# Performance work log

Hardware: AMD Instinct MI355X
Metric: run time of the kernel (lower is better)

Reference implementation:

```python
import jax, jax.numpy as jnp
import numpy as np

B, C, H, W, N = 4, 5, 256, 256, 2048
HW = H * W


def setup_inputs() -> dict:
    key = jax.random.key(0)
    ks = jax.random.split(key, 8)
    s = 1.0 / np.sqrt(C)
    x = jax.random.normal(ks[0], (B, C, H, W), jnp.float32)
    Wq = jax.random.normal(ks[1], (C, C), jnp.float32) * s
    Wk = jax.random.normal(ks[2], (C, C), jnp.float32) * s
    Wv = jax.random.normal(ks[3], (C, C), jnp.float32) * s
    bq = jnp.zeros((C,), jnp.float32)
    bk = jnp.zeros((C,), jnp.float32)
    bv = jnp.zeros((C,), jnp.float32)
    gamma = jnp.zeros((1,), jnp.float32)  # nn.Parameter(torch.zeros(1))
    idx_b = jax.random.randint(ks[4], (N,), 0, B, jnp.int32)
    idx_h = jax.random.randint(ks[5], (N,), 0, H, jnp.int32)
    idx_w = jax.random.randint(ks[6], (N,), 0, W, jnp.int32)
    return {"x": x, "Wq": Wq, "bq": bq, "Wk": Wk, "bk": bk, "Wv": Wv,
            "bv": bv, "gamma": gamma, "idx_b": idx_b, "idx_h": idx_h, "idx_w": idx_w}


def _conv1x1(x, Wt, b):
    # 1x1 conv == per-pixel channel mix
    return jnp.einsum('oc,bchw->bohw', Wt, x) + b[None, :, None, None]


def reference(x, Wq, bq, Wk, bk, Wv, bv, gamma, idx_b, idx_h, idx_w):
    q = _conv1x1(x, Wq, bq)
    k = _conv1x1(x, Wk, bk)
    v = _conv1x1(x, Wv, bv)
    q_pix = q[idx_b, :, idx_h, idx_w]              # [N, C] gathered query pixels
    Kf = k.reshape(B, C, HW)
    Vf = v.reshape(B, C, HW)
    # energy[n, l] = sum_c q_pix[n, c] * Kf[idx_b[n], c, l]
    # channel loop (C=5, fixed) avoids materializing [N, C, HW]
    energy = jnp.zeros((N, HW), x.dtype)
    for c in range(C):
        energy = energy + q_pix[:, c:c + 1] * Kf[idx_b, c]   # [N, HW]
    attn = jax.nn.softmax(energy, axis=-1)                   # [N, HW]
    out = jnp.stack([jnp.sum(Vf[idx_b, c] * attn, axis=-1) for c in range(C)],
                    axis=1)                                  # [N, C]
    upd = (gamma[0] + 0.1) * out + x[idx_b, :, idx_h, idx_w]
    # y starts as a detached copy of x; selected pixels are overwritten
    y = jax.lax.stop_gradient(x).at[idx_b, :, idx_h, idx_w].set(upd)
    return y
```

## Files before the change

kernel.cpp:

```cpp
#include <hip/hip_runtime.h>


constexpr int HWC = 256 * 256;
constexpr int Bc  = 4;
constexpr int Nq  = 2048;
constexpr int Wc  = 256;

constexpr int TPB   = 40;
constexpr int SPLIT = 16;

constexpr float LOG2E = 1.4426950408889634f;
constexpr float BIAS2 = -14.0f * LOG2E;

constexpr size_t K8_BYTES  = (size_t)Bc * HWC * 8 * 2;
constexpr size_t VT_BYTES  = (size_t)Bc * 5 * HWC * 2;
constexpr size_t QP_BYTES  = (size_t)Nq * 8 * 2;
constexpr size_t PART_BYTES = (size_t)SPLIT * Nq * 6 * 4;
constexpr size_t K8_OFF   = 0;
constexpr size_t VT_OFF   = K8_OFF + K8_BYTES;
constexpr size_t QP16_OFF = VT_OFF + VT_BYTES;
constexpr size_t PART_OFF = QP16_OFF + QP_BYTES;
constexpr size_t PERM_OFF = PART_OFF + PART_BYTES;
constexpr size_t CNT_OFF  = PERM_OFF + (size_t)Bc * Nq * 4;

typedef __attribute__((ext_vector_type(8))) _Float16 f16x8;
typedef __attribute__((ext_vector_type(4))) float f32x4;
union FU { uint4 u; f16x8 h; };

#if defined(__has_builtin)
#if __has_builtin(__builtin_amdgcn_exp2f)
#define EXP2F(x) __builtin_amdgcn_exp2f(x)
#endif
#endif
#ifndef EXP2F
#define EXP2F(x) exp2f(x)
#endif

__device__ inline unsigned pack2(float a, float b) {
  typedef __attribute__((ext_vector_type(2))) __fp16 fp16x2;
  union { fp16x2 h; unsigned u; } r;
  r.h = __builtin_amdgcn_cvt_pkrtz(a, b);
  return r.u;
}

__global__ __launch_bounds__(256) void k1_prep(
    const float* __restrict__ x,
    const float* __restrict__ Wq, const float* __restrict__ bq,
    const float* __restrict__ Wk, const float* __restrict__ bk,
    const float* __restrict__ Wv, const float* __restrict__ bv,
    const int* __restrict__ idx_b, const int* __restrict__ idx_h,
    const int* __restrict__ idx_w,
    float* __restrict__ y, char* __restrict__ wsb) {
  const int tid = threadIdx.x;
  _Float16* K8   = (_Float16*)(wsb + K8_OFF);
  _Float16* VT   = (_Float16*)(wsb + VT_OFF);
  _Float16* QP16 = (_Float16*)(wsb + QP16_OFF);
  if (blockIdx.x >= 1024) {
    if (blockIdx.x == 1032) {
      __shared__ int lcnt[Bc];
      if (tid < Bc) lcnt[tid] = 0;
      __syncthreads();
      int* perm = (int*)(wsb + PERM_OFF);
#pragma unroll
      for (int qi = 0; qi < 8; ++qi) {
        const int n = qi * 256 + tid;
        const int b = idx_b[n];
        const int pos = atomicAdd(&lcnt[b], 1);
        perm[b * Nq + pos] = n;
      }
      __syncthreads();
      if (tid < Bc) ((int*)(wsb + CNT_OFF))[tid] = lcnt[tid];
      return;
    }
    const int n = (blockIdx.x - 1024) * 256 + tid;
    const int b = idx_b[n];
    const int s = idx_h[n] * Wc + idx_w[n];
    float xv[5];
#pragma unroll
    for (int c = 0; c < 5; ++c) xv[c] = x[(size_t)(b * 5 + c) * HWC + s];
    float q[5];
#pragma unroll
    for (int o = 0; o < 5; ++o) {
      float t = bq[o];
#pragma unroll
      for (int c = 0; c < 5; ++c) t = fmaf(Wq[o * 5 + c], xv[c], t);
      q[o] = t * LOG2E;
    }
    uint4 row;
    row.x = pack2(q[0], q[1]);
    row.y = pack2(q[2], q[3]);
    row.z = pack2(q[4], 0.f);
    row.w = 0u;
    *(uint4*)(QP16 + (size_t)n * 8) = row;
    return;
  }
  const int gid = blockIdx.x * 256 + tid;
  const int b   = gid >> 16;
  const int s   = gid & (HWC - 1);
  float xv[5];
#pragma unroll
  for (int c = 0; c < 5; ++c) {
    const size_t off = (size_t)(b * 5 + c) * HWC + s;
    xv[c] = x[off];
    y[off] = xv[c];
  }
  float kk[5], vv[5];
#pragma unroll
  for (int o = 0; o < 5; ++o) {
    kk[o] = bk[o];
    vv[o] = bv[o];
#pragma unroll
    for (int c = 0; c < 5; ++c) {
      kk[o] = fmaf(Wk[o * 5 + c], xv[c], kk[o]);
      vv[o] = fmaf(Wv[o * 5 + c], xv[c], vv[o]);
    }
  }
  uint4 krow;
  krow.x = pack2(kk[0], kk[1]);
  krow.y = pack2(kk[2], kk[3]);
  krow.z = pack2(kk[4], 0.f);
  krow.w = 0u;
  *(uint4*)(K8 + (size_t)(b * HWC + s) * 8) = krow;
#pragma unroll
  for (int c = 0; c < 5; ++c)
    VT[(size_t)(b * 5 + c) * HWC + s] = (_Float16)vv[c];
}

#define BODY(KC0, KC1, KC2, KC3, KN0, KN1, KN2, KN3, VN0, VN1,                \
             NBASE, DOPV, DOLOAD, RPW, WPW)                                   \
  do {                                                                        \
    f32x4 e0 = __builtin_amdgcn_mfma_f32_16x16x32_f16(KC0.h, qf.h, bias, 0, 0, 0); \
    f32x4 e1 = __builtin_amdgcn_mfma_f32_16x16x32_f16(KC1.h, qf.h, bias, 0, 0, 0); \
    f32x4 e2 = __builtin_amdgcn_mfma_f32_16x16x32_f16(KC2.h, qf.h, bias, 0, 0, 0); \
    f32x4 e3 = __builtin_amdgcn_mfma_f32_16x16x32_f16(KC3.h, qf.h, bias, 0, 0, 0); \
    if (DOPV) {                                                               \
      FU pa0, pa1;                                                            \
      pa0.h = *(const f16x8*)((RPW) + roff0);                                 \
      pa1.h = *(const f16x8*)((RPW) + roff1);                                 \
      oacc = __builtin_amdgcn_mfma_f32_16x16x32_f16(pa0.h, VN0.h, oacc, 0, 0, 0); \
      oacc = __builtin_amdgcn_mfma_f32_16x16x32_f16(pa1.h, VN1.h, oacc, 0, 0, 0); \
    }                                                                         \
    if (DOLOAD) {                                                             \
      if (quad == 0) {                                                        \
        KN0.u = *(const uint4*)(K8b + (size_t)((NBASE) +  0 + l15) * 8);      \
        KN1.u = *(const uint4*)(K8b + (size_t)((NBASE) + 16 + l15) * 8);      \
        KN2.u = *(const uint4*)(K8b + (size_t)((NBASE) + 32 + l15) * 8);      \
        KN3.u = *(const uint4*)(K8b + (size_t)((NBASE) + 48 + l15) * 8);      \
      }                                                                       \
      if (l15 < 5) {                                                          \
        VN0.u = *(const uint4*)(vplane + (NBASE) +  0 + 8 * quad);            \
        VN1.u = *(const uint4*)(vplane + (NBASE) + 32 + 8 * quad);            \
      }                                                                       \
    }                                                                         \
    uint2 w0, w1, w2, w3;                                                     \
    w0.x = pack2(EXP2F(e0.x), EXP2F(e0.y)); w0.y = pack2(EXP2F(e0.z), EXP2F(e0.w)); \
    w1.x = pack2(EXP2F(e1.x), EXP2F(e1.y)); w1.y = pack2(EXP2F(e1.z), EXP2F(e1.w)); \
    w2.x = pack2(EXP2F(e2.x), EXP2F(e2.y)); w2.y = pack2(EXP2F(e2.z), EXP2F(e2.w)); \
    w3.x = pack2(EXP2F(e3.x), EXP2F(e3.y)); w3.y = pack2(EXP2F(e3.z), EXP2F(e3.w)); \
    *(uint2*)((WPW) + woff0) = w0;                                            \
    *(uint2*)((WPW) + woff1) = w1;                                            \
    *(uint2*)((WPW) + woff2) = w2;                                            \
    *(uint2*)((WPW) + woff3) = w3;                                            \
  } while (0)

__global__ __launch_bounds__(256, 4) void k2_attn(char* __restrict__ wsb) {
  const int chunk = blockIdx.x;
  const int tile  = blockIdx.y;
  const int bb    = tile / TPB;
  const int tt    = tile % TPB;
  const int cb    = ((const int*)(wsb + CNT_OFF))[bb];
  const int j0    = tt * 16;
  if (j0 >= cb) return;
  const int* perm = (const int*)(wsb + PERM_OFF) + bb * Nq;

  const int tid  = threadIdx.x;
  const int wv   = tid >> 6;
  const int lane = tid & 63;
  const int quad = lane >> 4;
  const int l15  = lane & 15;

  __shared__ _Float16 Pbuf[4][2][16][64];
  __shared__ float    Ored[4][16][6];

  const _Float16* K8b  = (const _Float16*)(wsb + K8_OFF) + (size_t)bb * HWC * 8;
  const _Float16* Vtb  = (const _Float16*)(wsb + VT_OFF) + (size_t)bb * 5 * HWC;
  const _Float16* QP16 = (const _Float16*)(wsb + QP16_OFF);

  _Float16* PwE = &Pbuf[wv][0][0][0];
  _Float16* PwO = &Pbuf[wv][1][0][0];
  const int swzg = 2 * (l15 & 7);
  const int rowb = l15 << 6;
  const int woff0 = rowb + (((0 * 4 + quad) ^ swzg) << 2);
  const int woff1 = rowb + (((1 * 4 + quad) ^ swzg) << 2);
  const int woff2 = rowb + (((2 * 4 + quad) ^ swzg) << 2);
  const int woff3 = rowb + (((3 * 4 + quad) ^ swzg) << 2);
  const int roff0 = rowb + (((0 + 2 * quad) ^ swzg) << 2);
  const int roff1 = rowb + (((8 + 2 * quad) ^ swzg) << 2);

  FU qf; qf.u = make_uint4(0u, 0u, 0u, 0u);
  {
    const int jq = j0 + l15;
    if (quad == 0) {
      const int n = (jq < cb) ? perm[jq] : 0;
      qf.u = *(const uint4*)(QP16 + (size_t)n * 8);
    }
  }
  FU vA0, vA1, vB0, vB1;
  {
    const unsigned ones = (l15 == 5) ? 0x3C003C00u : 0u;
    vA0.u = make_uint4(ones, ones, ones, ones);
    vA1.u = vA0.u; vB0.u = vA0.u; vB1.u = vA0.u;
  }
  FU kA0, kA1, kA2, kA3, kB0, kB1, kB2, kB3;
  kA0.u = make_uint4(0u, 0u, 0u, 0u);
  kA1.u = kA0.u; kA2.u = kA0.u; kA3.u = kA0.u;
  kB0.u = kA0.u; kB1.u = kA0.u; kB2.u = kA0.u; kB3.u = kA0.u;

  const f32x4 bias = {BIAS2, BIAS2, BIAS2, BIAS2};
  f32x4 oacc = {0.f, 0.f, 0.f, 0.f};

  const _Float16* vplane = Vtb + (size_t)l15 * HWC;

  const int s0 = chunk * (HWC / SPLIT) + wv * (HWC / SPLIT / 4);

  if (quad == 0) {
    kA0.u = *(const uint4*)(K8b + (size_t)(s0 +  0 + l15) * 8);
    kA1.u = *(const uint4*)(K8b + (size_t)(s0 + 16 + l15) * 8);
    kA2.u = *(const uint4*)(K8b + (size_t)(s0 + 32 + l15) * 8);
    kA3.u = *(const uint4*)(K8b + (size_t)(s0 + 48 + l15) * 8);
  }
  if (l15 < 5) {
    vA0.u = *(const uint4*)(vplane + s0 +  0);
    vA1.u = *(const uint4*)(vplane + s0 + 32);
  }
  if (l15 < 5 && quad != 0) {
    vA0.u = *(const uint4*)(vplane + s0 +  0 + 8 * quad);
    vA1.u = *(const uint4*)(vplane + s0 + 32 + 8 * quad);
  }

  BODY(kA0, kA1, kA2, kA3, kB0, kB1, kB2, kB3, vB0, vB1,
       s0 + 64, false, true, PwE, PwE);
#pragma unroll
  for (int p = 0; p < 7; ++p) {
    const int it = 1 + 2 * p;
    BODY(kB0, kB1, kB2, kB3, kA0, kA1, kA2, kA3, vA0, vA1,
         s0 + 64 * (it + 1), true, true, PwE, PwO);
    BODY(kA0, kA1, kA2, kA3, kB0, kB1, kB2, kB3, vB0, vB1,
         s0 + 64 * (it + 2), true, true, PwO, PwE);
  }
  BODY(kB0, kB1, kB2, kB3, kA0, kA1, kA2, kA3, vA0, vA1,
       0, true, false, PwE, PwO);
  {
    FU pa0, pa1;
    pa0.h = *(const f16x8*)(PwO + roff0);
    pa1.h = *(const f16x8*)(PwO + roff1);
    oacc = __builtin_amdgcn_mfma_f32_16x16x32_f16(pa0.h, vB0.h, oacc, 0, 0, 0);
    oacc = __builtin_amdgcn_mfma_f32_16x16x32_f16(pa1.h, vB1.h, oacc, 0, 0, 0);
  }

  if (l15 < 6) {
    Ored[wv][4 * quad + 0][l15] = oacc.x;
    Ored[wv][4 * quad + 1][l15] = oacc.y;
    Ored[wv][4 * quad + 2][l15] = oacc.z;
    Ored[wv][4 * quad + 3][l15] = oacc.w;
  }
  __syncthreads();
  if (tid < 96) {
    const int q = tid / 6, comp = tid % 6;
    const float s = Ored[0][q][comp] + Ored[1][q][comp] +
                    Ored[2][q][comp] + Ored[3][q][comp];
    const int j = j0 + q;
    if (j < cb) {
      const int n = perm[j];
      ((float*)(wsb + PART_OFF))[((size_t)chunk * Nq + n) * 6 + comp] = s;
    }
  }
}

__global__ __launch_bounds__(256) void k3_final(
    const float* __restrict__ x, const float* __restrict__ gamma,
    const int* __restrict__ idx_b, const int* __restrict__ idx_h,
    const int* __restrict__ idx_w, float* __restrict__ y,
    const char* __restrict__ wsb) {
  const int n = blockIdx.x * 256 + threadIdx.x;
  const float* part = (const float*)(wsb + PART_OFF);
  float l = 0.f, o[5] = {0.f, 0.f, 0.f, 0.f, 0.f};
#pragma unroll
  for (int ch = 0; ch < SPLIT; ++ch) {
    const float* p = part + ((size_t)ch * Nq + n) * 6;
#pragma unroll
    for (int c = 0; c < 5; ++c) o[c] += p[c];
    l += p[5];
  }
  const float gsc = gamma[0] + 0.1f;
  const float inv = 1.0f / l;
  const int b = idx_b[n], h = idx_h[n], w = idx_w[n];
  const int s = h * Wc + w;
#pragma unroll
  for (int c = 0; c < 5; ++c) {
    const size_t off = (size_t)(b * 5 + c) * HWC + s;
    y[off] = fmaf(gsc, o[c] * inv, x[off]);
  }
}

extern "C" void kernel_launch(void* const* d_in, const int* in_sizes, int n_in,
                              void* d_out, int out_size, void* d_ws, size_t ws_size,
                              hipStream_t stream) {
  const float* x     = (const float*)d_in[0];
  const float* Wq    = (const float*)d_in[1];
  const float* bq    = (const float*)d_in[2];
  const float* Wk    = (const float*)d_in[3];
  const float* bk    = (const float*)d_in[4];
  const float* Wv    = (const float*)d_in[5];
  const float* bv    = (const float*)d_in[6];
  const float* gamma = (const float*)d_in[7];
  const int* idx_b   = (const int*)d_in[8];
  const int* idx_h   = (const int*)d_in[9];
  const int* idx_w   = (const int*)d_in[10];
  float* y  = (float*)d_out;
  char* wsb = (char*)d_ws;

  k1_prep<<<1033, 256, 0, stream>>>(x, Wq, bq, Wk, bk, Wv, bv,
                                    idx_b, idx_h, idx_w, y, wsb);
  k2_attn<<<dim3(SPLIT, Bc * TPB), 256, 0, stream>>>(wsb);
  k3_final<<<Nq / 256, 256, 0, stream>>>(x, gamma, idx_b, idx_h, idx_w, y, wsb);
}
```

Baseline: 118.6 us.

## Process four query tiles per block to reuse each K/V load across 64 queries

Each attention block now handles 64 queries (four 16-query groups with separate accumulators) instead of 16. Every K and V fragment loaded from global memory is reused across four MFMA groups, cutting K/V traffic roughly fourfold. SPLIT doubles to 32 so the grid stays large enough to fill the GPU. The cost is more registers, longer serial work per block, and twice as many partial results for the final reduction kernel.

```diff
diff --git a/kernel.cpp b/kernel.cpp
--- a/kernel.cpp
+++ b/kernel.cpp
@@ -6,8 +6,8 @@
 constexpr int Nq  = 2048;
 constexpr int Wc  = 256;
 
-constexpr int TPB   = 40;
-constexpr int SPLIT = 16;
+constexpr int QG    = 10;
+constexpr int SPLIT = 32;
 
 constexpr float LOG2E = 1.4426950408889634f;
 constexpr float BIAS2 = -14.0f * LOG2E;
@@ -126,30 +126,32 @@
     VT[(size_t)(b * 5 + c) * HWC + s] = (_Float16)vv[c];
 }
 
-#define BODY(KC0, KC1, KC2, KC3, KN0, KN1, KN2, KN3, VN0, VN1,                \
-             NBASE, DOPV, DOLOAD, RPW, WPW)                                   \
+#define STEP(KC0, KC1, KC2, KC3, QF, DOPV, OACC, RPW, WPW,                    \
+             DOLV, VBASE, DOLK, KD0, KD1, KD2, KD3, KBASE)                    \
   do {                                                                        \
-    f32x4 e0 = __builtin_amdgcn_mfma_f32_16x16x32_f16(KC0.h, qf.h, bias, 0, 0, 0); \
-    f32x4 e1 = __builtin_amdgcn_mfma_f32_16x16x32_f16(KC1.h, qf.h, bias, 0, 0, 0); \
-    f32x4 e2 = __builtin_amdgcn_mfma_f32_16x16x32_f16(KC2.h, qf.h, bias, 0, 0, 0); \
-    f32x4 e3 = __builtin_amdgcn_mfma_f32_16x16x32_f16(KC3.h, qf.h, bias, 0, 0, 0); \
+    f32x4 e0 = __builtin_amdgcn_mfma_f32_16x16x32_f16(KC0.h, QF.h, bias, 0, 0, 0); \
+    f32x4 e1 = __builtin_amdgcn_mfma_f32_16x16x32_f16(KC1.h, QF.h, bias, 0, 0, 0); \
+    f32x4 e2 = __builtin_amdgcn_mfma_f32_16x16x32_f16(KC2.h, QF.h, bias, 0, 0, 0); \
+    f32x4 e3 = __builtin_amdgcn_mfma_f32_16x16x32_f16(KC3.h, QF.h, bias, 0, 0, 0); \
     if (DOPV) {                                                               \
       FU pa0, pa1;                                                            \
       pa0.h = *(const f16x8*)((RPW) + roff0);                                 \
       pa1.h = *(const f16x8*)((RPW) + roff1);                                 \
-      oacc = __builtin_amdgcn_mfma_f32_16x16x32_f16(pa0.h, VN0.h, oacc, 0, 0, 0); \
-      oacc = __builtin_amdgcn_mfma_f32_16x16x32_f16(pa1.h, VN1.h, oacc, 0, 0, 0); \
+      OACC = __builtin_amdgcn_mfma_f32_16x16x32_f16(pa0.h, v0.h, OACC, 0, 0, 0); \
+      OACC = __builtin_amdgcn_mfma_f32_16x16x32_f16(pa1.h, v1.h, OACC, 0, 0, 0); \
     }                                                                         \
-    if (DOLOAD) {                                                             \
+    if (DOLV) {                                                               \
+      if (l15 < 5) {                                                          \
+        v0.u = *(const uint4*)(vplane + (VBASE) +  0 + 8 * quad);             \
+        v1.u = *(const uint4*)(vplane + (VBASE) + 32 + 8 * quad);             \
+      }                                                                       \
+    }                                                                         \
+    if (DOLK) {                                                               \
       if (quad == 0) {                                                        \
-        KN0.u = *(const uint4*)(K8b + (size_t)((NBASE) +  0 + l15) * 8);      \
-        KN1.u = *(const uint4*)(K8b + (size_t)((NBASE) + 16 + l15) * 8);      \
-        KN2.u = *(const uint4*)(K8b + (size_t)((NBASE) + 32 + l15) * 8);      \
-        KN3.u = *(const uint4*)(K8b + (size_t)((NBASE) + 48 + l15) * 8);      \
-      }                                                                       \
-      if (l15 < 5) {                                                          \
-        VN0.u = *(const uint4*)(vplane + (NBASE) +  0 + 8 * quad);            \
-        VN1.u = *(const uint4*)(vplane + (NBASE) + 32 + 8 * quad);            \
+        KD0.u = *(const uint4*)(K8b + (size_t)((KBASE) +  0 + l15) * 8);      \
+        KD1.u = *(const uint4*)(K8b + (size_t)((KBASE) + 16 + l15) * 8);      \
+        KD2.u = *(const uint4*)(K8b + (size_t)((KBASE) + 32 + l15) * 8);      \
+        KD3.u = *(const uint4*)(K8b + (size_t)((KBASE) + 48 + l15) * 8);      \
       }                                                                       \
     }                                                                         \
     uint2 w0, w1, w2, w3;                                                     \
@@ -166,10 +168,10 @@
 __global__ __launch_bounds__(256, 4) void k2_attn(char* __restrict__ wsb) {
   const int chunk = blockIdx.x;
   const int tile  = blockIdx.y;
-  const int bb    = tile / TPB;
-  const int tt    = tile % TPB;
+  const int bb    = tile / QG;
+  const int tg    = tile % QG;
   const int cb    = ((const int*)(wsb + CNT_OFF))[bb];
-  const int j0    = tt * 16;
+  const int j0    = tg * 64;
   if (j0 >= cb) return;
   const int* perm = (const int*)(wsb + PERM_OFF) + bb * Nq;
 
@@ -180,7 +182,7 @@
   const int l15  = lane & 15;
 
   __shared__ _Float16 Pbuf[4][2][16][64];
-  __shared__ float    Ored[4][16][6];
+  __shared__ float    Ored[4][4][16][6];
 
   const _Float16* K8b  = (const _Float16*)(wsb + K8_OFF) + (size_t)bb * HWC * 8;
   const _Float16* Vtb  = (const _Float16*)(wsb + VT_OFF) + (size_t)bb * 5 * HWC;
@@ -197,19 +199,24 @@
   const int roff0 = rowb + (((0 + 2 * quad) ^ swzg) << 2);
   const int roff1 = rowb + (((8 + 2 * quad) ^ swzg) << 2);
 
-  FU qf; qf.u = make_uint4(0u, 0u, 0u, 0u);
-  {
-    const int jq = j0 + l15;
-    if (quad == 0) {
-      const int n = (jq < cb) ? perm[jq] : 0;
-      qf.u = *(const uint4*)(QP16 + (size_t)n * 8);
-    }
-  }
-  FU vA0, vA1, vB0, vB1;
+  FU qf0, qf1, qf2, qf3;
+  qf0.u = make_uint4(0u, 0u, 0u, 0u);
+  qf1.u = qf0.u; qf2.u = qf0.u; qf3.u = qf0.u;
+  if (quad == 0) {
+#define QLOAD(QF, G)                                                          \
+    do {                                                                      \
+      const int jq = j0 + 16 * (G) + l15;                                     \
+      const int n = (jq < cb) ? perm[jq] : 0;     \
+      QF.u = *(const uint4*)(QP16 + (size_t)n * 8);                           \
+    } while (0)
+    QLOAD(qf0, 0); QLOAD(qf1, 1); QLOAD(qf2, 2); QLOAD(qf3, 3);
+#undef QLOAD
+  }
+  FU v0, v1;
   {
     const unsigned ones = (l15 == 5) ? 0x3C003C00u : 0u;
-    vA0.u = make_uint4(ones, ones, ones, ones);
-    vA1.u = vA0.u; vB0.u = vA0.u; vB1.u = vA0.u;
+    v0.u = make_uint4(ones, ones, ones, ones);
+    v1.u = v0.u;
   }
   FU kA0, kA1, kA2, kA3, kB0, kB1, kB2, kB3;
   kA0.u = make_uint4(0u, 0u, 0u, 0u);
@@ -217,59 +224,90 @@
   kB0.u = kA0.u; kB1.u = kA0.u; kB2.u = kA0.u; kB3.u = kA0.u;
 
   const f32x4 bias = {BIAS2, BIAS2, BIAS2, BIAS2};
-  f32x4 oacc = {0.f, 0.f, 0.f, 0.f};
+  f32x4 oacc0 = {0.f, 0.f, 0.f, 0.f};
+  f32x4 oacc1 = oacc0, oacc2 = oacc0, oacc3 = oacc0;
 
   const _Float16* vplane = Vtb + (size_t)l15 * HWC;
 
-  const int s0 = chunk * (HWC / SPLIT) + wv * (HWC / SPLIT / 4);
+  const int s0w = chunk * (HWC / SPLIT) + wv * (HWC / SPLIT / 4);
 
   if (quad == 0) {
-    kA0.u = *(const uint4*)(K8b + (size_t)(s0 +  0 + l15) * 8);
-    kA1.u = *(const uint4*)(K8b + (size_t)(s0 + 16 + l15) * 8);
-    kA2.u = *(const uint4*)(K8b + (size_t)(s0 + 32 + l15) * 8);
-    kA3.u = *(const uint4*)(K8b + (size_t)(s0 + 48 + l15) * 8);
+    kA0.u = *(const uint4*)(K8b + (size_t)(s0w +  0 + l15) * 8);
+    kA1.u = *(const uint4*)(K8b + (size_t)(s0w + 16 + l15) * 8);
+    kA2.u = *(const uint4*)(K8b + (size_t)(s0w + 32 + l15) * 8);
+    kA3.u = *(const uint4*)(K8b + (size_t)(s0w + 48 + l15) * 8);
   }
   if (l15 < 5) {
-    vA0.u = *(const uint4*)(vplane + s0 +  0);
-    vA1.u = *(const uint4*)(vplane + s0 + 32);
-  }
-  if (l15 < 5 && quad != 0) {
-    vA0.u = *(const uint4*)(vplane + s0 +  0 + 8 * quad);
-    vA1.u = *(const uint4*)(vplane + s0 + 32 + 8 * quad);
-  }
-
-  BODY(kA0, kA1, kA2, kA3, kB0, kB1, kB2, kB3, vB0, vB1,
-       s0 + 64, false, true, PwE, PwE);
-#pragma unroll
-  for (int p = 0; p < 7; ++p) {
-    const int it = 1 + 2 * p;
-    BODY(kB0, kB1, kB2, kB3, kA0, kA1, kA2, kA3, vA0, vA1,
-         s0 + 64 * (it + 1), true, true, PwE, PwO);
-    BODY(kA0, kA1, kA2, kA3, kB0, kB1, kB2, kB3, vB0, vB1,
-         s0 + 64 * (it + 2), true, true, PwO, PwE);
-  }
-  BODY(kB0, kB1, kB2, kB3, kA0, kA1, kA2, kA3, vA0, vA1,
-       0, true, false, PwE, PwO);
+    v0.u = *(const uint4*)(vplane + s0w +  0 + 8 * quad);
+    v1.u = *(const uint4*)(vplane + s0w + 32 + 8 * quad);
+  }
+
+  STEP(kA0, kA1, kA2, kA3, qf0, false, oacc0, PwE, PwE,
+       false, 0, true, kB0, kB1, kB2, kB3, s0w + 64);
+  STEP(kA0, kA1, kA2, kA3, qf1, true, oacc0, PwE, PwO,
+       false, 0, false, kB0, kB1, kB2, kB3, 0);
+  STEP(kA0, kA1, kA2, kA3, qf2, true, oacc1, PwO, PwE,
+       false, 0, false, kB0, kB1, kB2, kB3, 0);
+  STEP(kA0, kA1, kA2, kA3, qf3, true, oacc2, PwE, PwO,
+       false, 0, false, kB0, kB1, kB2, kB3, 0);
+
+#pragma unroll
+  for (int p = 0; p < 3; ++p) {
+    const int ob = s0w + 64 * (2 * p + 1);
+    const int eb = s0w + 64 * (2 * p + 2);
+    const int nb = s0w + 64 * (2 * p + 3);
+    STEP(kB0, kB1, kB2, kB3, qf0, true, oacc3, PwO, PwE,
+         true, ob, true, kA0, kA1, kA2, kA3, eb);
+    STEP(kB0, kB1, kB2, kB3, qf1, true, oacc0, PwE, PwO,
+         false, 0, false, kA0, kA1, kA2, kA3, 0);
+    STEP(kB0, kB1, kB2, kB3, qf2, true, oacc1, PwO, PwE,
+         false, 0, false, kA0, kA1, kA2, kA3, 0);
+    STEP(kB0, kB1, kB2, kB3, qf3, true, oacc2, PwE, PwO,
+         false, 0, false, kA0, kA1, kA2, kA3, 0);
+    STEP(kA0, kA1, kA2, kA3, qf0, true, oacc3, PwO, PwE,
+         true, eb, true, kB0, kB1, kB2, kB3, nb);
+    STEP(kA0, kA1, kA2, kA3, qf1, true, oacc0, PwE, PwO,
+         false, 0, false, kB0, kB1, kB2, kB3, 0);
+    STEP(kA0, kA1, kA2, kA3, qf2, true, oacc1, PwO, PwE,
+         false, 0, false, kB0, kB1, kB2, kB3, 0);
+    STEP(kA0, kA1, kA2, kA3, qf3, true, oacc2, PwE, PwO,
+         false, 0, false, kB0, kB1, kB2, kB3, 0);
+  }
+
+  STEP(kB0, kB1, kB2, kB3, qf0, true, oacc3, PwO, PwE,
+       true, s0w + 64 * 7, false, kA0, kA1, kA2, kA3, 0);
+  STEP(kB0, kB1, kB2, kB3, qf1, true, oacc0, PwE, PwO,
+       false, 0, false, kA0, kA1, kA2, kA3, 0);
+  STEP(kB0, kB1, kB2, kB3, qf2, true, oacc1, PwO, PwE,
+       false, 0, false, kA0, kA1, kA2, kA3, 0);
+  STEP(kB0, kB1, kB2, kB3, qf3, true, oacc2, PwE, PwO,
+       false, 0, false, kA0, kA1, kA2, kA3, 0);
   {
     FU pa0, pa1;
     pa0.h = *(const f16x8*)(PwO + roff0);
     pa1.h = *(const f16x8*)(PwO + roff1);
-    oacc = __builtin_amdgcn_mfma_f32_16x16x32_f16(pa0.h, vB0.h, oacc, 0, 0, 0);
-    oacc = __builtin_amdgcn_mfma_f32_16x16x32_f16(pa1.h, vB1.h, oacc, 0, 0, 0);
+    oacc3 = __builtin_amdgcn_mfma_f32_16x16x32_f16(pa0.h, v0.h, oacc3, 0, 0, 0);
+    oacc3 = __builtin_amdgcn_mfma_f32_16x16x32_f16(pa1.h, v1.h, oacc3, 0, 0, 0);
   }
 
   if (l15 < 6) {
-    Ored[wv][4 * quad + 0][l15] = oacc.x;
-    Ored[wv][4 * quad + 1][l15] = oacc.y;
-    Ored[wv][4 * quad + 2][l15] = oacc.z;
-    Ored[wv][4 * quad + 3][l15] = oacc.w;
+#define OSTORE(G, OA)                                                         \
+    do {                                                                      \
+      Ored[wv][G][4 * quad + 0][l15] = OA.x;                                  \
+      Ored[wv][G][4 * quad + 1][l15] = OA.y;                                  \
+      Ored[wv][G][4 * quad + 2][l15] = OA.z;                                  \
+      Ored[wv][G][4 * quad + 3][l15] = OA.w;                                  \
+    } while (0)
+    OSTORE(0, oacc0); OSTORE(1, oacc1); OSTORE(2, oacc2); OSTORE(3, oacc3);
+#undef OSTORE
   }
   __syncthreads();
-  if (tid < 96) {
-    const int q = tid / 6, comp = tid % 6;
-    const float s = Ored[0][q][comp] + Ored[1][q][comp] +
-                    Ored[2][q][comp] + Ored[3][q][comp];
-    const int j = j0 + q;
+  for (int o = tid; o < 64 * 6; o += 256) {
+    const int q64 = o / 6, comp = o % 6;
+    const int g = q64 >> 4, q16 = q64 & 15;
+    const float s = Ored[0][g][q16][comp] + Ored[1][g][q16][comp] +
+                    Ored[2][g][q16][comp] + Ored[3][g][q16][comp];
+    const int j = j0 + q64;
     if (j < cb) {
       const int n = perm[j];
       ((float*)(wsb + PART_OFF))[((size_t)chunk * Nq + n) * 6 + comp] = s;
@@ -322,6 +360,6 @@
 
   k1_prep<<<1033, 256, 0, stream>>>(x, Wq, bq, Wk, bk, Wv, bv,
                                     idx_b, idx_h, idx_w, y, wsb);
-  k2_attn<<<dim3(SPLIT, Bc * TPB), 256, 0, stream>>>(wsb);
+  k2_attn<<<dim3(SPLIT, Bc * QG), 256, 0, stream>>>(wsb);
   k3_final<<<Nq / 256, 256, 0, stream>>>(x, gamma, idx_b, idx_h, idx_w, y, wsb);
 }
```

New measurement: 108.6 us. 1.09x faster.
